# Performance work log

Measured on AMD Instinct MI355X. Metric: run time of the kernel, lower is better.

The kernel has to match this reference:

```python
import jax, jax.numpy as jnp
import numpy as np

TOP_K = 8
ROUTE_SCALE = 2.5
NUM_EXPERTS = 64


def setup_inputs() -> dict:
    key = jax.random.key(0)
    k1, k2, k3 = jax.random.split(key, 3)
    x = jax.random.normal(k1, (16384, 4096), dtype=jnp.float32)
    gate_weight = jax.random.normal(k2, (NUM_EXPERTS, 4096), dtype=jnp.float32) * 0.02
    expert_bias = jax.random.normal(k3, (NUM_EXPERTS,), dtype=jnp.float32) * 0.01
    return {"x": x, "gate_weight": gate_weight, "expert_bias": expert_bias}


def reference(x, gate_weight, expert_bias):
    # gate linear: [T, dim] @ [dim, E] -> [T, E]
    logits = jnp.einsum("td,ed->te", x, gate_weight)
    scores = jax.nn.sigmoid(logits.astype(jnp.float32))  # score_func == 'sigmoid'
    # expert_bias branch: top-k over biased scores, gather unbiased scores
    _, selected_experts_indices = jax.lax.top_k(scores + expert_bias[None, :], TOP_K)
    top_scores = jnp.take_along_axis(scores, selected_experts_indices, axis=1)
    # route_norm (sigmoid normalization)
    denom = top_scores.sum(axis=-1, keepdims=True) + 1e-20
    top_scores = top_scores / denom * ROUTE_SCALE
    # histogram over selected expert indices (torch.histc returns float)
    flat_idx = selected_experts_indices.reshape(-1)
    num_tokens_per_expert = jnp.zeros((NUM_EXPERTS,), jnp.float32).at[flat_idx].add(1.0)
    return top_scores, selected_experts_indices, num_tokens_per_expert
```

## Files before the change

### kernel.cpp

```cpp
#include <hip/hip_runtime.h>
#include <math.h>

#define NTOK 16384
#define DIM  4096
#define NE   64
#define TOPK 8
#define TPB  32
#define CHUNK 128
#define NCH  (DIM / CHUNK)
#define ROUTE_SCALE 2.5f

typedef __attribute__((ext_vector_type(8))) short short8v;
typedef __attribute__((ext_vector_type(4))) float f32x4;

__device__ __forceinline__ void split3_pack(const float* v, uint4& b0, uint4& b1, uint4& b2)
{
    uint p0[8], p1[8], p2[8];
#pragma unroll
    for (int j = 0; j < 8; ++j) {
        const float xv = v[j];
        const uint  u0 = __float_as_uint(xv) & 0xffff0000u;
        const float f0 = __uint_as_float(u0);
        const float r  = xv - f0;
        const uint  u1 = __float_as_uint(r) & 0xffff0000u;
        const float f1 = __uint_as_float(u1);
        const float r2 = r - f1;
        const uint  u2 = __float_as_uint(r2) & 0xffff0000u;
        p0[j] = u0; p1[j] = u1; p2[j] = u2;
    }
    b0 = make_uint4(p0[1] | (p0[0] >> 16), p0[3] | (p0[2] >> 16),
                    p0[5] | (p0[4] >> 16), p0[7] | (p0[6] >> 16));
    b1 = make_uint4(p1[1] | (p1[0] >> 16), p1[3] | (p1[2] >> 16),
                    p1[5] | (p1[4] >> 16), p1[7] | (p1[6] >> 16));
    b2 = make_uint4(p2[1] | (p2[0] >> 16), p2[3] | (p2[2] >> 16),
                    p2[5] | (p2[4] >> 16), p2[7] | (p2[6] >> 16));
}

__device__ __forceinline__ void split3_pack4(const float4 v, uint2& q0, uint2& q1, uint2& q2)
{
    const float vv[4] = {v.x, v.y, v.z, v.w};
    uint p0[4], p1[4], p2[4];
#pragma unroll
    for (int j = 0; j < 4; ++j) {
        const float xv = vv[j];
        const uint  u0 = __float_as_uint(xv) & 0xffff0000u;
        const float f0 = __uint_as_float(u0);
        const float r  = xv - f0;
        const uint  u1 = __float_as_uint(r) & 0xffff0000u;
        const float f1 = __uint_as_float(u1);
        const float r2 = r - f1;
        const uint  u2 = __float_as_uint(r2) & 0xffff0000u;
        p0[j] = u0; p1[j] = u1; p2[j] = u2;
    }
    q0 = make_uint2(p0[1] | (p0[0] >> 16), p0[3] | (p0[2] >> 16));
    q1 = make_uint2(p1[1] | (p1[0] >> 16), p1[3] | (p1[2] >> 16));
    q2 = make_uint2(p2[1] | (p2[0] >> 16), p2[3] | (p2[2] >> 16));
}

__global__ __launch_bounds__(256)
void prep_w(const float* __restrict__ gw, uint4* __restrict__ wS)
{
    const int tid  = blockIdx.x * 256 + threadIdx.x;
    const int lane = tid & 63;
    const int nt   = (tid >> 6) & 3;
    const int ks   = tid >> 8;
    const int e    = nt * 16 + (lane & 15);
    const int kb   = ks * 32 + (lane >> 4) * 8;
    float v[8];
    *(float4*)&v[0] = *(const float4*)&gw[(size_t)e * DIM + kb];
    *(float4*)&v[4] = *(const float4*)&gw[(size_t)e * DIM + kb + 4];
    uint4 b0, b1, b2;
    split3_pack(v, b0, b1, b2);
    const size_t base = (size_t)(ks * 4 + nt) * 3 * 64 + lane;
    wS[base] = b0; wS[base + 64] = b1; wS[base + 128] = b2;
}

#define MFMA6(A0, A1, A2, B0, B1, B2, ACC) do {                              \
    ACC = __builtin_amdgcn_mfma_f32_16x16x32_bf16(A2, B0, ACC, 0, 0, 0);     \
    ACC = __builtin_amdgcn_mfma_f32_16x16x32_bf16(A1, B1, ACC, 0, 0, 0);     \
    ACC = __builtin_amdgcn_mfma_f32_16x16x32_bf16(A0, B2, ACC, 0, 0, 0);     \
    ACC = __builtin_amdgcn_mfma_f32_16x16x32_bf16(A1, B0, ACC, 0, 0, 0);     \
    ACC = __builtin_amdgcn_mfma_f32_16x16x32_bf16(A0, B1, ACC, 0, 0, 0);     \
    ACC = __builtin_amdgcn_mfma_f32_16x16x32_bf16(A0, B0, ACC, 0, 0, 0);     \
} while (0)

__global__ __launch_bounds__(256, 2)
void router_fused(const float* __restrict__ x, const uint4* __restrict__ wS,
                  const float* __restrict__ bias, float* __restrict__ out)
{
    __shared__ ushort xp[2][3][TPB][CHUNK];
    __shared__ float  sc[TPB][NE + 1];
    __shared__ int    hist[NE];

    const int t    = threadIdx.x;
    const int lane = t & 63;
    const int wv   = __builtin_amdgcn_readfirstlane(t >> 6);
    const int r15  = lane & 15;
    const int g    = lane >> 4;
    const int tok0 = blockIdx.x * TPB;

    if (t < NE) hist[t] = 0;

    const int srow = t >> 3;
    const int sg   = t & 7;
    const float* xsrc = x + (size_t)(tok0 + srow) * DIM + sg * 4;

    const uint4* wB = wS + wv * 192 + lane;

    f32x4 acc0 = {0.f, 0.f, 0.f, 0.f};
    f32x4 acc1 = {0.f, 0.f, 0.f, 0.f};
    uint4  B0[12], B1[12];
    float4 stP[4], stQ[4];

#define STAGE_LOAD(ST, c1) do {                                              \
        _Pragma("unroll")                                                    \
        for (int j = 0; j < 4; ++j)                                          \
            ST[j] = *(const float4*)(xsrc + (size_t)(c1) * CHUNK + j * 32);  \
    } while (0)

#define STAGE_WRITE(ST, bb) do {                                             \
        _Pragma("unroll")                                                    \
        for (int j = 0; j < 4; ++j) {                                        \
            uint2 q0, q1, q2;                                                \
            split3_pack4(ST[j], q0, q1, q2);                                 \
            const int gg  = sg + 8 * j;                                      \
            const int off = (((gg >> 1) ^ (srow & 15)) << 3) + ((gg & 1) << 2); \
            *(uint2*)&xp[bb][0][srow][off] = q0;                             \
            *(uint2*)&xp[bb][1][srow][off] = q1;                             \
            *(uint2*)&xp[bb][2][srow][off] = q2;                             \
        }                                                                    \
    } while (0)

#define LOADB(B, c1) do {                                                    \
        _Pragma("unroll")                                                    \
        for (int s2 = 0; s2 < 4; ++s2)                                       \
            _Pragma("unroll")                                                \
            for (int sp = 0; sp < 3; ++sp)                                   \
                B[s2 * 3 + sp] = wB[(size_t)((c1) * 4 + s2) * 768 + sp * 64];\
    } while (0)

#define SLICE(B, cb, s) do {                                                 \
        const int off = ((((s) * 4 + g) ^ r15) << 3);                        \
        const short8v a0_0 = *(const short8v*)&xp[cb][0][r15][off];          \
        const short8v a1_0 = *(const short8v*)&xp[cb][1][r15][off];          \
        const short8v a2_0 = *(const short8v*)&xp[cb][2][r15][off];          \
        const short8v a0_1 = *(const short8v*)&xp[cb][0][16 + r15][off];     \
        const short8v a1_1 = *(const short8v*)&xp[cb][1][16 + r15][off];     \
        const short8v a2_1 = *(const short8v*)&xp[cb][2][16 + r15][off];     \
        const short8v b0 = *(const short8v*)&B[(s) * 3 + 0];                 \
        const short8v b1 = *(const short8v*)&B[(s) * 3 + 1];                 \
        const short8v b2 = *(const short8v*)&B[(s) * 3 + 2];                 \
        MFMA6(a0_0, a1_0, a2_0, b0, b1, b2, acc0);                           \
        MFMA6(a0_1, a1_1, a2_1, b0, b1, b2, acc1);                           \
    } while (0)

#define CHUNK_BODY(c, BU, BV, STW, STL) do {                                 \
        __syncthreads();                                                     \
        SLICE(BU, (c) & 1, 0);                                               \
        SLICE(BU, (c) & 1, 1);                                               \
        SLICE(BU, (c) & 1, 2);                                               \
        SLICE(BU, (c) & 1, 3);                                               \
        if ((c) + 1 < NCH) { LOADB(BV, (c) + 1); STAGE_WRITE(STW, ((c) & 1) ^ 1); } \
        if ((c) + 2 < NCH) { STAGE_LOAD(STL, (c) + 2); }                     \
    } while (0)

    LOADB(B0, 0);
    STAGE_LOAD(stP, 0);
    STAGE_WRITE(stP, 0);
    STAGE_LOAD(stP, 1);

    for (int c = 0; c < NCH; c += 2) {
        CHUNK_BODY(c,     B0, B1, stP, stQ);
        CHUNK_BODY(c + 1, B1, B0, stQ, stP);
    }
#undef STAGE_LOAD
#undef STAGE_WRITE
#undef LOADB
#undef SLICE
#undef CHUNK_BODY

#pragma unroll
    for (int q = 0; q < 4; ++q) {
        sc[g * 4 + q][wv * 16 + r15]      = 1.f / (1.f + expf(-acc0[q]));
        sc[16 + g * 4 + q][wv * 16 + r15] = 1.f / (1.f + expf(-acc1[q]));
    }
    __syncthreads();

    const float bias_l = bias[lane];
#pragma unroll 1
    for (int i = 0; i < 8; ++i) {
        const int tok = wv * 8 + i;
        const float s = sc[tok][lane];
        float myv  = s + bias_l;
        float outv = 0.f;
        int   outi = 0;
        float sum  = 0.f;
#pragma unroll
        for (int k = 0; k < TOPK; ++k) {
            float cv = myv;
            int   ci = lane;
#pragma unroll
            for (int off = 32; off; off >>= 1) {
                float ov = __shfl_xor(cv, off, 64);
                int   oi = __shfl_xor(ci, off, 64);
                if (ov > cv || (ov == cv && oi < ci)) { cv = ov; ci = oi; }
            }
            float ts = __shfl(s, ci, 64);
            sum += ts;
            if (lane == k)  { outv = ts; outi = ci; }
            if (lane == ci) { myv = -1e30f; }
        }
        const float denom = sum + 1e-20f;
        const size_t gt = (size_t)tok0 + tok;
        if (lane < TOPK) {
            out[gt * TOPK + lane] = (outv / denom) * ROUTE_SCALE;
            out[(size_t)NTOK * TOPK + gt * TOPK + lane] = (float)outi;
            atomicAdd(&hist[outi], 1);
        }
    }

    __syncthreads();
    if (t < NE) {
        int cgt = hist[t];
        if (cgt) atomicAdd(&out[(size_t)NTOK * TOPK * 2 + t], (float)cgt);
    }
}

extern "C" void kernel_launch(void* const* d_in, const int* in_sizes, int n_in,
                              void* d_out, int out_size, void* d_ws, size_t ws_size,
                              hipStream_t stream)
{
    const float* x    = (const float*)d_in[0];
    const float* gw   = (const float*)d_in[1];
    const float* bias = (const float*)d_in[2];
    float* out = (float*)d_out;
    uint4* wS  = (uint4*)d_ws;

    hipMemsetAsync(out + (size_t)NTOK * TOPK * 2, 0, NE * sizeof(float), stream);

    prep_w<<<128, 256, 0, stream>>>(gw, wS);
    router_fused<<<NTOK / TPB, 256, 0, stream>>>(x, wS, bias, out);
}
```

Before: 112.4 us.

## Stream x tiles to LDS via direct global-to-LDS loads with 5-stage ring

```diff
diff --git a/kernel.cpp b/kernel.cpp
--- a/kernel.cpp
+++ b/kernel.cpp
@@ -6,8 +6,9 @@
 #define NE   64
 #define TOPK 8
 #define TPB  32
-#define CHUNK 128
+#define CHUNK 64
 #define NCH  (DIM / CHUNK)
+#define NB   5
 #define ROUTE_SCALE 2.5f
 
 typedef __attribute__((ext_vector_type(8))) short short8v;
@@ -34,27 +35,6 @@
                     p1[5] | (p1[4] >> 16), p1[7] | (p1[6] >> 16));
     b2 = make_uint4(p2[1] | (p2[0] >> 16), p2[3] | (p2[2] >> 16),
                     p2[5] | (p2[4] >> 16), p2[7] | (p2[6] >> 16));
-}
-
-__device__ __forceinline__ void split3_pack4(const float4 v, uint2& q0, uint2& q1, uint2& q2)
-{
-    const float vv[4] = {v.x, v.y, v.z, v.w};
-    uint p0[4], p1[4], p2[4];
-#pragma unroll
-    for (int j = 0; j < 4; ++j) {
-        const float xv = vv[j];
-        const uint  u0 = __float_as_uint(xv) & 0xffff0000u;
-        const float f0 = __uint_as_float(u0);
-        const float r  = xv - f0;
-        const uint  u1 = __float_as_uint(r) & 0xffff0000u;
-        const float f1 = __uint_as_float(u1);
-        const float r2 = r - f1;
-        const uint  u2 = __float_as_uint(r2) & 0xffff0000u;
-        p0[j] = u0; p1[j] = u1; p2[j] = u2;
-    }
-    q0 = make_uint2(p0[1] | (p0[0] >> 16), p0[3] | (p0[2] >> 16));
-    q1 = make_uint2(p1[1] | (p1[0] >> 16), p1[3] | (p1[2] >> 16));
-    q2 = make_uint2(p2[1] | (p2[0] >> 16), p2[3] | (p2[2] >> 16));
 }
 
 __global__ __launch_bounds__(256)
@@ -75,6 +55,14 @@
     wS[base] = b0; wS[base + 64] = b1; wS[base + 128] = b2;
 }
 
+__device__ __forceinline__ void gld_lds16(const float* g, float* l)
+{
+    __builtin_amdgcn_global_load_lds(
+        (const __attribute__((address_space(1))) unsigned int*)g,
+        (__attribute__((address_space(3))) unsigned int*)l,
+        16, 0, 0);
+}
+
 #define MFMA6(A0, A1, A2, B0, B1, B2, ACC) do {                              \
     ACC = __builtin_amdgcn_mfma_f32_16x16x32_bf16(A2, B0, ACC, 0, 0, 0);     \
     ACC = __builtin_amdgcn_mfma_f32_16x16x32_bf16(A1, B1, ACC, 0, 0, 0);     \
@@ -84,13 +72,20 @@
     ACC = __builtin_amdgcn_mfma_f32_16x16x32_bf16(A0, B0, ACC, 0, 0, 0);     \
 } while (0)
 
-__global__ __launch_bounds__(256, 2)
+#define FENCE   asm volatile("" ::: "memory")
+#define WAITV(N) do { asm volatile("s_waitcnt vmcnt(" #N ")" ::: "memory"); \
+                      __builtin_amdgcn_sched_barrier(0); } while (0)
+#define BAR     do { __builtin_amdgcn_sched_barrier(0);                     \
+                     __builtin_amdgcn_s_barrier();                          \
+                     __builtin_amdgcn_sched_barrier(0); } while (0)
+
+__global__ __launch_bounds__(256)
 void router_fused(const float* __restrict__ x, const uint4* __restrict__ wS,
                   const float* __restrict__ bias, float* __restrict__ out)
 {
-    __shared__ ushort xp[2][3][TPB][CHUNK];
-    __shared__ float  sc[TPB][NE + 1];
-    __shared__ int    hist[NE];
+    __shared__ float raw[NB][TPB][CHUNK];
+    __shared__ float sc[TPB][NE + 1];
+    __shared__ int   hist[NE];
 
     const int t    = threadIdx.x;
     const int lane = t & 63;
@@ -101,83 +96,94 @@
 
     if (t < NE) hist[t] = 0;
 
-    const int srow = t >> 3;
-    const int sg   = t & 7;
-    const float* xsrc = x + (size_t)(tok0 + srow) * DIM + sg * 4;
-
-    const uint4* wB = wS + wv * 192 + lane;
+    const int r0  = (wv * 2 + 0) * 4 + (lane >> 4);
+    const int r1  = (wv * 2 + 1) * 4 + (lane >> 4);
+    const int gl0 = (lane & 15) ^ (r0 & 15);
+    const int gl1 = (lane & 15) ^ (r1 & 15);
+    const float* gsrc0 = x + (size_t)(tok0 + r0) * DIM + gl0 * 4;
+    const float* gsrc1 = x + (size_t)(tok0 + r1) * DIM + gl1 * 4;
+    float* ldst0 = &raw[0][(wv * 2 + 0) * 4][0];
+    float* ldst1 = &raw[0][(wv * 2 + 1) * 4][0];
+
+    const uint4* wB = wS + (size_t)wv * 192 + lane;
 
     f32x4 acc0 = {0.f, 0.f, 0.f, 0.f};
     f32x4 acc1 = {0.f, 0.f, 0.f, 0.f};
-    uint4  B0[12], B1[12];
-    float4 stP[4], stQ[4];
-
-#define STAGE_LOAD(ST, c1) do {                                              \
-        _Pragma("unroll")                                                    \
-        for (int j = 0; j < 4; ++j)                                          \
-            ST[j] = *(const float4*)(xsrc + (size_t)(c1) * CHUNK + j * 32);  \
-    } while (0)
-
-#define STAGE_WRITE(ST, bb) do {                                             \
-        _Pragma("unroll")                                                    \
-        for (int j = 0; j < 4; ++j) {                                        \
-            uint2 q0, q1, q2;                                                \
-            split3_pack4(ST[j], q0, q1, q2);                                 \
-            const int gg  = sg + 8 * j;                                      \
-            const int off = (((gg >> 1) ^ (srow & 15)) << 3) + ((gg & 1) << 2); \
-            *(uint2*)&xp[bb][0][srow][off] = q0;                             \
-            *(uint2*)&xp[bb][1][srow][off] = q1;                             \
-            *(uint2*)&xp[bb][2][srow][off] = q2;                             \
-        }                                                                    \
-    } while (0)
-
+    uint4 Bev[6], Bod[6];
+
+#define DMA2(c, b) do {                                                      \
+        gld_lds16(gsrc0 + (size_t)(c) * CHUNK, ldst0 + (size_t)(b) * TPB * CHUNK); \
+        gld_lds16(gsrc1 + (size_t)(c) * CHUNK, ldst1 + (size_t)(b) * TPB * CHUNK); \
+    } while (0)
 #define LOADB(B, c1) do {                                                    \
         _Pragma("unroll")                                                    \
-        for (int s2 = 0; s2 < 4; ++s2)                                       \
+        for (int s2 = 0; s2 < 2; ++s2)                                       \
             _Pragma("unroll")                                                \
             for (int sp = 0; sp < 3; ++sp)                                   \
-                B[s2 * 3 + sp] = wB[(size_t)((c1) * 4 + s2) * 768 + sp * 64];\
-    } while (0)
-
-#define SLICE(B, cb, s) do {                                                 \
-        const int off = ((((s) * 4 + g) ^ r15) << 3);                        \
-        const short8v a0_0 = *(const short8v*)&xp[cb][0][r15][off];          \
-        const short8v a1_0 = *(const short8v*)&xp[cb][1][r15][off];          \
-        const short8v a2_0 = *(const short8v*)&xp[cb][2][r15][off];          \
-        const short8v a0_1 = *(const short8v*)&xp[cb][0][16 + r15][off];     \
-        const short8v a1_1 = *(const short8v*)&xp[cb][1][16 + r15][off];     \
-        const short8v a2_1 = *(const short8v*)&xp[cb][2][16 + r15][off];     \
-        const short8v b0 = *(const short8v*)&B[(s) * 3 + 0];                 \
-        const short8v b1 = *(const short8v*)&B[(s) * 3 + 1];                 \
-        const short8v b2 = *(const short8v*)&B[(s) * 3 + 2];                 \
-        MFMA6(a0_0, a1_0, a2_0, b0, b1, b2, acc0);                           \
-        MFMA6(a0_1, a1_1, a2_1, b0, b1, b2, acc1);                           \
-    } while (0)
-
-#define CHUNK_BODY(c, BU, BV, STW, STL) do {                                 \
-        __syncthreads();                                                     \
-        SLICE(BU, (c) & 1, 0);                                               \
-        SLICE(BU, (c) & 1, 1);                                               \
-        SLICE(BU, (c) & 1, 2);                                               \
-        SLICE(BU, (c) & 1, 3);                                               \
-        if ((c) + 1 < NCH) { LOADB(BV, (c) + 1); STAGE_WRITE(STW, ((c) & 1) ^ 1); } \
-        if ((c) + 2 < NCH) { STAGE_LOAD(STL, (c) + 2); }                     \
-    } while (0)
-
-    LOADB(B0, 0);
-    STAGE_LOAD(stP, 0);
-    STAGE_WRITE(stP, 0);
-    STAGE_LOAD(stP, 1);
-
-    for (int c = 0; c < NCH; c += 2) {
-        CHUNK_BODY(c,     B0, B1, stP, stQ);
-        CHUNK_BODY(c + 1, B1, B0, stQ, stP);
-    }
-#undef STAGE_LOAD
-#undef STAGE_WRITE
+                B[s2 * 3 + sp] = wB[(size_t)(2 * (c1) + s2) * 768 + sp * 64];\
+    } while (0)
+#define SLICE_C(rp, B, s) do {                                               \
+        const int gA = (s) * 8 + g * 2;                                      \
+        float a8[8]; uint4 a0u, a1u, a2u;                                    \
+        *(float4*)&a8[0] = *(const float4*)(rp + r15 * CHUNK + (gA ^ r15) * 4);        \
+        *(float4*)&a8[4] = *(const float4*)(rp + r15 * CHUNK + ((gA + 1) ^ r15) * 4);  \
+        split3_pack(a8, a0u, a1u, a2u);                                      \
+        MFMA6(*(short8v*)&a0u, *(short8v*)&a1u, *(short8v*)&a2u,             \
+              *(const short8v*)&B[(s)*3+0], *(const short8v*)&B[(s)*3+1],    \
+              *(const short8v*)&B[(s)*3+2], acc0);                           \
+        *(float4*)&a8[0] = *(const float4*)(rp + (16 + r15) * CHUNK + (gA ^ r15) * 4);       \
+        *(float4*)&a8[4] = *(const float4*)(rp + (16 + r15) * CHUNK + ((gA + 1) ^ r15) * 4); \
+        split3_pack(a8, a0u, a1u, a2u);                                      \
+        MFMA6(*(short8v*)&a0u, *(short8v*)&a1u, *(short8v*)&a2u,             \
+              *(const short8v*)&B[(s)*3+0], *(const short8v*)&B[(s)*3+1],    \
+              *(const short8v*)&B[(s)*3+2], acc1);                           \
+    } while (0)
+#define COMPCHUNK(bix, B) do {                                               \
+        const float* rp = &raw[bix][0][0];                                   \
+        SLICE_C(rp, B, 0);                                                   \
+        SLICE_C(rp, B, 1);                                                   \
+    } while (0)
+
+    DMA2(0, 0); FENCE;
+    DMA2(1, 1); FENCE;
+    DMA2(2, 2); FENCE;
+    DMA2(3, 3);
+    LOADB(Bev, 0);
+
+    int bi = 0, bd = 4;
+    WAITV(12); BAR;
+    DMA2(4, bd); bd = 0;
+    LOADB(Bod, 1);
+    COMPCHUNK(bi, Bev); bi = 1;
+    WAITV(18); BAR;
+    DMA2(5, bd); bd = 1;
+    LOADB(Bev, 2);
+    COMPCHUNK(bi, Bod); bi = 2;
+#pragma unroll 1
+    for (int i = 2; i < 60; i += 2) {
+        WAITV(24); BAR;
+        DMA2(i + 4, bd); bd = (bd == NB - 1) ? 0 : bd + 1;
+        LOADB(Bod, i + 1);
+        COMPCHUNK(bi, Bev); bi = (bi == NB - 1) ? 0 : bi + 1;
+        WAITV(24); BAR;
+        DMA2(i + 5, bd); bd = (bd == NB - 1) ? 0 : bd + 1;
+        LOADB(Bev, i + 2);
+        COMPCHUNK(bi, Bod); bi = (bi == NB - 1) ? 0 : bi + 1;
+    }
+    WAITV(24); BAR;
+    LOADB(Bod, 61);
+    COMPCHUNK(bi, Bev); bi = (bi == NB - 1) ? 0 : bi + 1;
+    WAITV(0); BAR;
+    LOADB(Bev, 62);
+    COMPCHUNK(bi, Bod); bi = (bi == NB - 1) ? 0 : bi + 1;
+    LOADB(Bod, 63);
+    COMPCHUNK(bi, Bev); bi = (bi == NB - 1) ? 0 : bi + 1;
+    COMPCHUNK(bi, Bod);
+
+#undef DMA2
 #undef LOADB
-#undef SLICE
-#undef CHUNK_BODY
+#undef SLICE_C
+#undef COMPCHUNK
 
 #pragma unroll
     for (int q = 0; q < 4; ++q) {
```

New measurement: 153.1 us. +36.2%, slower.
